# Performance work log

Measured on AMD Instinct MI355X. Metric: run time of the kernel, lower is better.

## Reference

```python
import jax, jax.numpy as jnp
import numpy as np

NUM_STEPS = 3
NUM_POINTS = 16
IN_CHANNELS = 64
OUT_CHANNELS = 256


def setup_inputs() -> dict:
    key = jax.random.key(0)
    k1, k2, k3 = jax.random.split(key, 3)
    data = jax.random.normal(k1, (4096, IN_CHANNELS), dtype=jnp.float32)
    # nn.Parameter(2*rand - 1): uniform in [-1, 1]
    angles = 2.0 * jax.random.uniform(k2, (NUM_POINTS,), dtype=jnp.float32) - 1.0
    velo = 2.0 * jax.random.uniform(k3, (NUM_POINTS,), dtype=jnp.float32) - 1.0
    return {"data": data, "angles": angles, "velo": velo}


def reference(data, angles, velo):
    # broadcast to [N, in_channels, out_channels] (data.view(-1,C,1) * ones(1,1,O))
    x = data.reshape(-1, IN_CHANNELS, 1) * jnp.ones((1, 1, OUT_CHANNELS), dtype=data.dtype)

    def step(x):
        t = jnp.tanh(x)
        # tanh-quantized bin index; clip keeps the edge bin in range
        # (torch would index OOB when round hits num_points; jax clamps anyway)
        pos = jnp.clip(
            jnp.round((1.0 + t) * (NUM_POINTS / 2.0)).astype(jnp.int32),
            0, NUM_POINTS - 1,
        )
        v = velo[pos]      # tiny 16-entry LUT gathers
        a = angles[pos]
        return v * jnp.cos(a) + t * v * jnp.sin(a)

    for _ in range(NUM_STEPS):
        x = x + step(x) / NUM_STEPS

    # sum over in_channels -> [N, out_channels]
    return jnp.sum(x, axis=1)
```

## Files before the change

### kernel.cpp

```cpp
#include <hip/hip_runtime.h>
#include <math.h>

#define NUM_STEPS   3
#define NUM_POINTS  16
#define IN_CH       64
#define OUT_CH      256

__global__ __launch_bounds__(256)
void flow_kernel(const float* __restrict__ data,
                 const float* __restrict__ angles,
                 const float* __restrict__ velo,
                 float* __restrict__ out,
                 int nrows) {
    __shared__ float s_vcos[NUM_POINTS];
    __shared__ float s_vsin[NUM_POINTS];

    const int tid = threadIdx.x;
    if (tid < NUM_POINTS) {
        const float a = angles[tid];
        const float v = velo[tid];
        s_vcos[tid] = v * cosf(a);
        s_vsin[tid] = v * sinf(a);
    }
    __syncthreads();

    const int lane = tid & 63;
    const int wave = tid >> 6;
    const int row  = blockIdx.x * (blockDim.x >> 6) + wave;
    if (row >= nrows) return;

    float x = data[row * IN_CH + lane];

#pragma unroll
    for (int s = 0; s < NUM_STEPS; ++s) {
        const float t = tanhf(x);
        int pos = (int)rintf((1.0f + t) * (NUM_POINTS * 0.5f));
        pos = min(max(pos, 0), NUM_POINTS - 1);
        const float st = s_vcos[pos] + t * s_vsin[pos];
        x += st / (float)NUM_STEPS;
    }

#pragma unroll
    for (int off = 1; off < 64; off <<= 1) {
        x += __shfl_xor(x, off);
    }

    float4 v4 = make_float4(x, x, x, x);
    reinterpret_cast<float4*>(out + (size_t)row * OUT_CH)[lane] = v4;
}

extern "C" void kernel_launch(void* const* d_in, const int* in_sizes, int n_in,
                              void* d_out, int out_size, void* d_ws, size_t ws_size,
                              hipStream_t stream) {
    const float* data   = (const float*)d_in[0];
    const float* angles = (const float*)d_in[1];
    const float* velo   = (const float*)d_in[2];
    float* out = (float*)d_out;

    const int nrows = in_sizes[0] / IN_CH;
    const int rows_per_block = 256 / 64;
    const int grid = (nrows + rows_per_block - 1) / rows_per_block;

    flow_kernel<<<grid, 256, 0, stream>>>(data, angles, velo, out, nrows);
}
```

Measured before the change: 9.756 us.

## Process four channels per thread with float4 loads and 16-lane row reduction

Each thread now loads a float4 of input channels and runs the three-step flow update on all four, so each row is handled by 16 lanes instead of a full wave. The cross-lane reduction shrinks to four shuffle stages, and each thread writes four float4 outputs. The grid becomes four times smaller, which cuts launch and reduction overhead and widens memory accesses, but leaves fewer waves to hide latency.

```diff
diff --git a/kernel.cpp b/kernel.cpp
--- a/kernel.cpp
+++ b/kernel.cpp
@@ -7,10 +7,10 @@
 #define OUT_CH      256
 
 __global__ __launch_bounds__(256)
-void flow_kernel(const float* __restrict__ data,
+void flow_kernel(const float4* __restrict__ data4,
                  const float* __restrict__ angles,
                  const float* __restrict__ velo,
-                 float* __restrict__ out,
+                 float4* __restrict__ out4,
                  int nrows) {
     __shared__ float s_vcos[NUM_POINTS];
     __shared__ float s_vsin[NUM_POINTS];
@@ -24,29 +24,39 @@
     }
     __syncthreads();
 
-    const int lane = tid & 63;
-    const int wave = tid >> 6;
-    const int row  = blockIdx.x * (blockDim.x >> 6) + wave;
+    const int gidx = blockIdx.x * 256 + tid;
+    const int row  = gidx >> 4;
+    const int cg   = gidx & 15;
     if (row >= nrows) return;
 
-    float x = data[row * IN_CH + lane];
+    const float4 xv = data4[gidx];
+    float xs[4] = {xv.x, xv.y, xv.z, xv.w};
 
+    float part = 0.0f;
 #pragma unroll
-    for (int s = 0; s < NUM_STEPS; ++s) {
-        const float t = tanhf(x);
-        int pos = (int)rintf((1.0f + t) * (NUM_POINTS * 0.5f));
-        pos = min(max(pos, 0), NUM_POINTS - 1);
-        const float st = s_vcos[pos] + t * s_vsin[pos];
-        x += st / (float)NUM_STEPS;
+    for (int k = 0; k < 4; ++k) {
+        float x = xs[k];
+#pragma unroll
+        for (int s = 0; s < NUM_STEPS; ++s) {
+            const float t = tanhf(x);
+            int pos = (int)rintf((1.0f + t) * (NUM_POINTS * 0.5f));
+            pos = min(max(pos, 0), NUM_POINTS - 1);
+            const float st = s_vcos[pos] + t * s_vsin[pos];
+            x += st / (float)NUM_STEPS;
+        }
+        part += x;
     }
 
 #pragma unroll
-    for (int off = 1; off < 64; off <<= 1) {
-        x += __shfl_xor(x, off);
+    for (int off = 1; off < 16; off <<= 1) {
+        part += __shfl_xor(part, off);
     }
 
-    float4 v4 = make_float4(x, x, x, x);
-    reinterpret_cast<float4*>(out + (size_t)row * OUT_CH)[lane] = v4;
+    const float4 v4 = make_float4(part, part, part, part);
+#pragma unroll
+    for (int k = 0; k < 4; ++k) {
+        out4[(size_t)row * (OUT_CH / 4) + cg + 16 * k] = v4;
+    }
 }
 
 extern "C" void kernel_launch(void* const* d_in, const int* in_sizes, int n_in,
@@ -58,8 +68,9 @@
     float* out = (float*)d_out;
 
     const int nrows = in_sizes[0] / IN_CH;
-    const int rows_per_block = 256 / 64;
-    const int grid = (nrows + rows_per_block - 1) / rows_per_block;
+    const int total_threads = nrows * (IN_CH / 4);
+    const int grid = (total_threads + 255) / 256;
 
-    flow_kernel<<<grid, 256, 0, stream>>>(data, angles, velo, out, nrows);
+    flow_kernel<<<grid, 256, 0, stream>>>(
+        (const float4*)data, angles, velo, (float4*)out, nrows);
 }
```

Measured after the change: 9.816 us. No clear change (+0.6%).
